# Kernel tuning notes

Measured on AMD Instinct MI355X. Metric: run time of the kernel, lower is better.

Reference implementation:

```python
import jax, jax.numpy as jnp
import numpy as np

DIM = 256
NUM_HEADS = 8
HEAD_DIM = DIM // NUM_HEADS
SCALE = float(HEAD_DIM) ** (-0.5)


def setup_inputs() -> dict:
    key = jax.random.key(0)
    ks = jax.random.split(key, 11)
    TGT, B = 2048, 4
    q = jax.random.normal(ks[0], (TGT, B, DIM), dtype=jnp.float32)
    k = jax.random.normal(ks[1], (TGT, B, DIM), dtype=jnp.float32)
    v = jax.random.normal(ks[2], (TGT, B, DIM), dtype=jnp.float32)
    init = 1.0 / np.sqrt(DIM)
    Wq = jax.random.uniform(ks[3], (DIM, DIM), jnp.float32, -init, init)
    bq = jax.random.uniform(ks[4], (DIM,), jnp.float32, -init, init)
    Wk = jax.random.uniform(ks[5], (DIM, DIM), jnp.float32, -init, init)
    bk = jax.random.uniform(ks[6], (DIM,), jnp.float32, -init, init)
    Wv = jax.random.uniform(ks[7], (DIM, DIM), jnp.float32, -init, init)
    bv = jax.random.uniform(ks[8], (DIM,), jnp.float32, -init, init)
    Wp = jax.random.uniform(ks[9], (DIM, DIM), jnp.float32, -init, init)
    bp = jax.random.uniform(ks[10], (DIM,), jnp.float32, -init, init)
    return {"q": q, "k": k, "v": v, "Wq": Wq, "bq": bq, "Wk": Wk, "bk": bk,
            "Wv": Wv, "bv": bv, "Wp": Wp, "bp": bp}


def reference(q, k, v, Wq, bq, Wk, bk, Wv, bv, Wp, bp):
    tgt_len, bsz, embed_dim = q.shape
    src_len = k.shape[0]
    # NOTE: original scales q BEFORE the q projection (faithful to source).
    qp = (q * SCALE) @ Wq.T + bq                      # [T, B, D]
    kp = k @ Wk.T + bk                                # [S, B, D]
    vp = v @ Wv.T + bv                                # [S, B, D]
    # reshape to (B*H, len, head_dim) like view + transpose(0,1)
    qh = qp.reshape(tgt_len, bsz * NUM_HEADS, HEAD_DIM).transpose(1, 0, 2)
    kh = kp.reshape(src_len, bsz * NUM_HEADS, HEAD_DIM).transpose(1, 0, 2)
    vh = vp.reshape(src_len, bsz * NUM_HEADS, HEAD_DIM).transpose(1, 0, 2)
    attn = jnp.einsum('bqd,bkd->bqk', qh, kh)         # [B*H, T, S]
    attn = jax.nn.softmax(attn, axis=-1)
    out = jnp.einsum('bqk,bkd->bqd', attn, vh)        # [B*H, T, hd]
    out = out.transpose(1, 0, 2).reshape(tgt_len, bsz, embed_dim)
    out = out @ Wp.T + bp                             # output projection
    return out
```

## Files before the change

### kernel.cpp

```cpp
#include <hip/hip_runtime.h>
#include <hip/hip_bf16.h>

#define T_LEN 2048
#define BSZ 4
#define EMB 256
#define HDIM 32
#define QSCALE 0.17677669529663687f
#define LOG2E 1.4426950408889634f

using bf16x8 = __attribute__((ext_vector_type(8))) short;
using bf16x4 = __attribute__((ext_vector_type(4))) short;
using f32x4 = __attribute__((ext_vector_type(4))) float;

static __device__ __forceinline__ unsigned fasu(float f) {
  union { float f; unsigned u; } c; c.f = f; return c.u;
}
static __device__ __forceinline__ unsigned pack2r(float lo, float hi) {
  return __builtin_amdgcn_perm(fasu(hi) + 0x8000u, fasu(lo) + 0x8000u, 0x07060302u);
}
static __device__ __forceinline__ unsigned short bfr(float x) {
  return (unsigned short)((fasu(x) + 0x8000u) >> 16);
}

__global__ __launch_bounds__(256) void cvt_w4(const float* __restrict__ s0, const float* __restrict__ s1,
                                              const float* __restrict__ s2, const float* __restrict__ s3,
                                              unsigned* __restrict__ d0, unsigned* __restrict__ d1,
                                              unsigned* __restrict__ d2, unsigned* __restrict__ d3) {
  const float* src = blockIdx.y == 0 ? s0 : blockIdx.y == 1 ? s1 : blockIdx.y == 2 ? s2 : s3;
  unsigned* dst = blockIdx.y == 0 ? d0 : blockIdx.y == 1 ? d1 : blockIdx.y == 2 ? d2 : d3;
  int i = blockIdx.x * 256 + threadIdx.x;
  float4 v = ((const float4*)src)[i];
  uint2 o; o.x = pack2r(v.x, v.y); o.y = pack2r(v.z, v.w);
  ((uint2*)dst)[i] = o;
}

__global__ __launch_bounds__(256) void qkv_proj(
    const float* __restrict__ Aq, const float* __restrict__ Ak, const float* __restrict__ Av,
    const unsigned short* __restrict__ Wq, const unsigned short* __restrict__ Wk, const unsigned short* __restrict__ Wv,
    const float* __restrict__ bq, const float* __restrict__ bk, const float* __restrict__ bv,
    unsigned short* __restrict__ qh, unsigned short* __restrict__ kh, unsigned short* __restrict__ vt) {
  __shared__ __align__(16) unsigned short smem[64 * 72];
  const int z = blockIdx.z;
  const float* A = z == 0 ? Aq : z == 1 ? Ak : Av;
  const unsigned short* W = z == 0 ? Wq : z == 1 ? Wk : Wv;
  const float* bias = z == 0 ? bq : z == 1 ? bk : bv;
  const float ascale = z == 0 ? QSCALE * LOG2E : 1.0f;
  const float bscale = z == 0 ? LOG2E : 1.0f;
  const int lane = threadIdx.x & 63;
  const int wave = threadIdx.x >> 6;
  const int quad = lane >> 4;
  const int l16 = lane & 15;
  const int m0b = blockIdx.x * 64;
  const int m0 = m0b + wave * 16;
  const int n0 = blockIdx.y * 64;
  f32x4 acc0 = {0.f, 0.f, 0.f, 0.f}, acc1 = acc0, acc2 = acc0, acc3 = acc0;
  const float* arow = A + (m0 + l16) * EMB;
#pragma unroll
  for (int k0 = 0; k0 < EMB; k0 += 32) {
    const float4* ap = (const float4*)(arow + k0 + quad * 8);
    float4 a0 = ap[0], a1 = ap[1];
    union { unsigned u[4]; bf16x8 v; } af;
    af.u[0] = pack2r(a0.x * ascale, a0.y * ascale);
    af.u[1] = pack2r(a0.z * ascale, a0.w * ascale);
    af.u[2] = pack2r(a1.x * ascale, a1.y * ascale);
    af.u[3] = pack2r(a1.z * ascale, a1.w * ascale);
    const unsigned short* wbase = W + k0 + quad * 8;
    bf16x8 b0 = *(const bf16x8*)(wbase + (n0 + 0 + l16) * EMB);
    bf16x8 b1 = *(const bf16x8*)(wbase + (n0 + 16 + l16) * EMB);
    bf16x8 b2 = *(const bf16x8*)(wbase + (n0 + 32 + l16) * EMB);
    bf16x8 b3 = *(const bf16x8*)(wbase + (n0 + 48 + l16) * EMB);
    acc0 = __builtin_amdgcn_mfma_f32_16x16x32_bf16(af.v, b0, acc0, 0, 0, 0);
    acc1 = __builtin_amdgcn_mfma_f32_16x16x32_bf16(af.v, b1, acc1, 0, 0, 0);
    acc2 = __builtin_amdgcn_mfma_f32_16x16x32_bf16(af.v, b2, acc2, 0, 0, 0);
    acc3 = __builtin_amdgcn_mfma_f32_16x16x32_bf16(af.v, b3, acc3, 0, 0, 0);
  }
  f32x4 accs[4] = {acc0, acc1, acc2, acc3};
#pragma unroll
  for (int nt = 0; nt < 4; ++nt) {
    float bn = bias[n0 + nt * 16 + l16] * bscale;
#pragma unroll
    for (int r = 0; r < 4; ++r)
      smem[(wave * 16 + quad * 4 + r) * 72 + nt * 16 + l16] = bfr(accs[nt][r] + bn);
  }
  __syncthreads();
  if (z < 2) {
    int row = threadIdx.x >> 2, seg = threadIdx.x & 3;
    int m = m0b + row, t = m >> 2, b = m & 3;
    int n = n0 + seg * 16, h = n >> 5, hd = n & 31;
    unsigned short* dst = (z == 0 ? qh : kh) + (((b << 3) + h) * T_LEN + t) * HDIM + hd;
    *(bf16x8*)(dst + 0) = *(const bf16x8*)(smem + row * 72 + seg * 16 + 0);
    *(bf16x8*)(dst + 8) = *(const bf16x8*)(smem + row * 72 + seg * 16 + 8);
  } else {
    int n = threadIdx.x >> 2, b = threadIdx.x & 3;
    unsigned w[8];
#pragma unroll
    for (int i = 0; i < 8; ++i) {
      unsigned lo = smem[((2 * i) * 4 + b) * 72 + n];
      unsigned hi = smem[((2 * i + 1) * 4 + b) * 72 + n];
      w[i] = lo | (hi << 16);
    }
    int nf = n0 + n, h = nf >> 5, hd = nf & 31;
    int tbase = m0b >> 2;
    unsigned* base = (unsigned*)(vt + (((b << 3) + h) * HDIM + hd) * T_LEN + tbase);
    ((uint4*)base)[0] = make_uint4(w[0], w[1], w[2], w[3]);
    ((uint4*)base)[1] = make_uint4(w[4], w[5], w[6], w[7]);
  }
}

__global__ __launch_bounds__(256) void out_gemm(const unsigned short* __restrict__ A,
                                                const unsigned short* __restrict__ W,
                                                const float* __restrict__ bias,
                                                float* __restrict__ out) {
  __shared__ __align__(16) float smem[64 * 68];
  const int lane = threadIdx.x & 63;
  const int wave = threadIdx.x >> 6;
  const int quad = lane >> 4;
  const int l16 = lane & 15;
  const int m0b = blockIdx.x * 64;
  const int m0 = m0b + wave * 16;
  const int n0 = blockIdx.y * 64;
  f32x4 acc0 = {0.f, 0.f, 0.f, 0.f}, acc1 = acc0, acc2 = acc0, acc3 = acc0;
  const unsigned short* arow = A + (m0 + l16) * EMB;
#pragma unroll
  for (int k0 = 0; k0 < EMB; k0 += 32) {
    bf16x8 af = *(const bf16x8*)(arow + k0 + quad * 8);
    const unsigned short* wbase = W + k0 + quad * 8;
    bf16x8 b0 = *(const bf16x8*)(wbase + (n0 + 0 + l16) * EMB);
    bf16x8 b1 = *(const bf16x8*)(wbase + (n0 + 16 + l16) * EMB);
    bf16x8 b2 = *(const bf16x8*)(wbase + (n0 + 32 + l16) * EMB);
    bf16x8 b3 = *(const bf16x8*)(wbase + (n0 + 48 + l16) * EMB);
    acc0 = __builtin_amdgcn_mfma_f32_16x16x32_bf16(af, b0, acc0, 0, 0, 0);
    acc1 = __builtin_amdgcn_mfma_f32_16x16x32_bf16(af, b1, acc1, 0, 0, 0);
    acc2 = __builtin_amdgcn_mfma_f32_16x16x32_bf16(af, b2, acc2, 0, 0, 0);
    acc3 = __builtin_amdgcn_mfma_f32_16x16x32_bf16(af, b3, acc3, 0, 0, 0);
  }
  f32x4 accs[4] = {acc0, acc1, acc2, acc3};
#pragma unroll
  for (int nt = 0; nt < 4; ++nt) {
    float bn = bias[n0 + nt * 16 + l16];
#pragma unroll
    for (int r = 0; r < 4; ++r)
      smem[(wave * 16 + quad * 4 + r) * 68 + nt * 16 + l16] = accs[nt][r] + bn;
  }
  __syncthreads();
  int row = threadIdx.x >> 2, seg = threadIdx.x & 3;
  const float4* srcp = (const float4*)(smem + row * 68 + seg * 16);
  float4* dstp = (float4*)(out + (m0b + row) * EMB + n0 + seg * 16);
#pragma unroll
  for (int i = 0; i < 4; ++i) dstp[i] = srcp[i];
}

__global__ __launch_bounds__(256) void flash_attn(const unsigned short* __restrict__ qh,
                                                  const unsigned short* __restrict__ kh,
                                                  const unsigned short* __restrict__ vt,
                                                  unsigned short* __restrict__ aout) {
  __shared__ __align__(16) unsigned short kbuf[2][128 * 32];
  __shared__ __align__(16) unsigned short vbuf[2][32 * 136];
  const int tid = threadIdx.x;
  const int lane = tid & 63;
  const int wave = tid >> 6;
  const int quad = lane >> 4;
  const int l16 = lane & 15;
  const int bh = blockIdx.x;
  const int q0 = blockIdx.y * 128 + wave * 32;
  const unsigned short* qs = qh + bh * (T_LEN * HDIM);
  const unsigned short* ks = kh + bh * (T_LEN * HDIM);
  const unsigned short* vs = vt + bh * (T_LEN * HDIM);
  const bf16x8 qf0 = *(const bf16x8*)(qs + (q0 + l16) * HDIM + quad * 8);
  const bf16x8 qf1 = *(const bf16x8*)(qs + (q0 + 16 + l16) * HDIM + quad * 8);
  f32x4 o00 = {0.f, 0.f, 0.f, 0.f};
  f32x4 o01 = o00, o10 = o00, o11 = o00, la0 = o00, la1 = o00;
  const f32x4 zero = o00;
  bf16x4 ones;
  ones[0] = ones[1] = ones[2] = ones[3] = (short)0x3F80;

  const int vrow = tid >> 4;
  const int vcol = (tid & 15) * 8;

  {
    uint4 ka = *(const uint4*)(ks + tid * 8);
    uint4 kb = *(const uint4*)(ks + (tid + 256) * 8);
    uint4 va = *(const uint4*)(vs + vrow * T_LEN + vcol);
    uint4 vb = *(const uint4*)(vs + (vrow + 16) * T_LEN + vcol);
    *(uint4*)(&kbuf[0][tid * 8]) = ka;
    *(uint4*)(&kbuf[0][(tid + 256) * 8]) = kb;
    *(uint4*)(&vbuf[0][vrow * 136 + vcol]) = va;
    *(uint4*)(&vbuf[0][(vrow + 16) * 136 + vcol]) = vb;
  }
  __syncthreads();

  for (int chunk = 0; chunk < 16; ++chunk) {
    const int buf = chunk & 1;
    uint4 ka, kb, va, vb;
    const bool pf = (chunk + 1) < 16;
    if (pf) {
      const int kk0 = (chunk + 1) * 128;
      const unsigned short* kg = ks + kk0 * HDIM;
      ka = *(const uint4*)(kg + tid * 8);
      kb = *(const uint4*)(kg + (tid + 256) * 8);
      va = *(const uint4*)(vs + vrow * T_LEN + kk0 + vcol);
      vb = *(const uint4*)(vs + (vrow + 16) * T_LEN + kk0 + vcol);
    }
#pragma unroll
    for (int it = 0; it < 8; ++it) {
      const int kkl = it * 16;
      bf16x8 kf = *(const bf16x8*)(&kbuf[buf][(kkl + l16) * 32 + quad * 8]);
      bf16x4 vfa = *(const bf16x4*)(&vbuf[buf][l16 * 136 + kkl + quad * 4]);
      bf16x4 vfb = *(const bf16x4*)(&vbuf[buf][(l16 + 16) * 136 + kkl + quad * 4]);
      f32x4 s0 = __builtin_amdgcn_mfma_f32_16x16x32_bf16(kf, qf0, zero, 0, 0, 0);
      f32x4 s1 = __builtin_amdgcn_mfma_f32_16x16x32_bf16(kf, qf1, zero, 0, 0, 0);
      union { unsigned u[2]; bf16x4 v; } pp0, pp1;
      {
        float a = __builtin_amdgcn_exp2f(s0[0]), b = __builtin_amdgcn_exp2f(s0[1]);
        float c = __builtin_amdgcn_exp2f(s0[2]), d = __builtin_amdgcn_exp2f(s0[3]);
        pp0.u[0] = pack2r(a, b); pp0.u[1] = pack2r(c, d);
        a = __builtin_amdgcn_exp2f(s1[0]); b = __builtin_amdgcn_exp2f(s1[1]);
        c = __builtin_amdgcn_exp2f(s1[2]); d = __builtin_amdgcn_exp2f(s1[3]);
        pp1.u[0] = pack2r(a, b); pp1.u[1] = pack2r(c, d);
      }
      o00 = __builtin_amdgcn_mfma_f32_16x16x16bf16_1k(vfa, pp0.v, o00, 0, 0, 0);
      o01 = __builtin_amdgcn_mfma_f32_16x16x16bf16_1k(vfb, pp0.v, o01, 0, 0, 0);
      la0 = __builtin_amdgcn_mfma_f32_16x16x16bf16_1k(ones, pp0.v, la0, 0, 0, 0);
      o10 = __builtin_amdgcn_mfma_f32_16x16x16bf16_1k(vfa, pp1.v, o10, 0, 0, 0);
      o11 = __builtin_amdgcn_mfma_f32_16x16x16bf16_1k(vfb, pp1.v, o11, 0, 0, 0);
      la1 = __builtin_amdgcn_mfma_f32_16x16x16bf16_1k(ones, pp1.v, la1, 0, 0, 0);
    }
    if (pf) {
      const int nb = buf ^ 1;
      *(uint4*)(&kbuf[nb][tid * 8]) = ka;
      *(uint4*)(&kbuf[nb][(tid + 256) * 8]) = kb;
      *(uint4*)(&vbuf[nb][vrow * 136 + vcol]) = va;
      *(uint4*)(&vbuf[nb][(vrow + 16) * 136 + vcol]) = vb;
    }
    __syncthreads();
  }

  const int srcA = l16 + ((quad & 1) << 5);
  const int srcB = srcA + 16;
  const bool lowq = quad < 2;
  const int b = bh >> 3, h = bh & 7;
#pragma unroll
  for (int f = 0; f < 2; ++f) {
    f32x4 oh0 = f == 0 ? o00 : o10;
    f32x4 oh1 = f == 0 ? o01 : o11;
    const float inv = 1.f / (f == 0 ? la0[0] : la1[0]);
    unsigned oa = pack2r(oh0[0] * inv, oh0[1] * inv), ob = pack2r(oh0[2] * inv, oh0[3] * inv);
    unsigned oc = pack2r(oh1[0] * inv, oh1[1] * inv), od = pack2r(oh1[2] * inv, oh1[3] * inv);
    union { unsigned u[4]; bf16x8 v; } of;
    unsigned ta, tc;
    ta = __shfl(oa, srcA); tc = __shfl(oc, srcA); of.u[0] = lowq ? ta : tc;
    ta = __shfl(ob, srcA); tc = __shfl(od, srcA); of.u[1] = lowq ? ta : tc;
    ta = __shfl(oa, srcB); tc = __shfl(oc, srcB); of.u[2] = lowq ? ta : tc;
    ta = __shfl(ob, srcB); tc = __shfl(od, srcB); of.u[3] = lowq ? ta : tc;
    const int t = q0 + f * 16 + l16;
    *(bf16x8*)(aout + (t * BSZ + b) * EMB + h * HDIM + quad * 8) = of.v;
  }
}

extern "C" void kernel_launch(void* const* d_in, const int* in_sizes, int n_in,
                              void* d_out, int out_size, void* d_ws, size_t ws_size,
                              hipStream_t stream) {
  const float* q  = (const float*)d_in[0];
  const float* k  = (const float*)d_in[1];
  const float* v  = (const float*)d_in[2];
  const float* Wq = (const float*)d_in[3];
  const float* bq = (const float*)d_in[4];
  const float* Wk = (const float*)d_in[5];
  const float* bk = (const float*)d_in[6];
  const float* Wv = (const float*)d_in[7];
  const float* bv = (const float*)d_in[8];
  const float* Wp = (const float*)d_in[9];
  const float* bp = (const float*)d_in[10];
  float* out = (float*)d_out;

  char* ws = (char*)d_ws;
  unsigned short* qh   = (unsigned short*)(ws);
  unsigned short* kh   = (unsigned short*)(ws + (4u << 20));
  unsigned short* vt   = (unsigned short*)(ws + (8u << 20));
  unsigned short* aout = (unsigned short*)(ws + (12u << 20));
  unsigned short* wqb  = (unsigned short*)(ws + (16u << 20));
  unsigned short* wkb  = wqb + 65536;
  unsigned short* wvb  = wqb + 2 * 65536;
  unsigned short* wpb  = wqb + 3 * 65536;

  cvt_w4<<<dim3(64, 4), 256, 0, stream>>>(Wq, Wk, Wv, Wp,
                                          (unsigned*)wqb, (unsigned*)wkb,
                                          (unsigned*)wvb, (unsigned*)wpb);
  qkv_proj<<<dim3(128, 4, 3), 256, 0, stream>>>(q, k, v, wqb, wkb, wvb, bq, bk, bv, qh, kh, vt);
  flash_attn<<<dim3(32, 16), 256, 0, stream>>>(qh, kh, vt, aout);
  out_gemm<<<dim3(128, 4), 256, 0, stream>>>(aout, wpb, bp, out);
}
```

Measured before the change: 166.8 us.

## Split attention over key halves and add a combine kernel

```diff
diff --git a/kernel.cpp b/kernel.cpp
--- a/kernel.cpp
+++ b/kernel.cpp
@@ -153,7 +153,8 @@
 __global__ __launch_bounds__(256) void flash_attn(const unsigned short* __restrict__ qh,
                                                   const unsigned short* __restrict__ kh,
                                                   const unsigned short* __restrict__ vt,
-                                                  unsigned short* __restrict__ aout) {
+                                                  float* __restrict__ po,
+                                                  float* __restrict__ pl) {
   __shared__ __align__(16) unsigned short kbuf[2][128 * 32];
   __shared__ __align__(16) unsigned short vbuf[2][32 * 136];
   const int tid = threadIdx.x;
@@ -162,7 +163,9 @@
   const int quad = lane >> 4;
   const int l16 = lane & 15;
   const int bh = blockIdx.x;
+  const int split = blockIdx.z;
   const int q0 = blockIdx.y * 128 + wave * 32;
+  const int kbeg = split * 1024;
   const unsigned short* qs = qh + bh * (T_LEN * HDIM);
   const unsigned short* ks = kh + bh * (T_LEN * HDIM);
   const unsigned short* vs = vt + bh * (T_LEN * HDIM);
@@ -178,10 +181,11 @@
   const int vcol = (tid & 15) * 8;
 
   {
-    uint4 ka = *(const uint4*)(ks + tid * 8);
-    uint4 kb = *(const uint4*)(ks + (tid + 256) * 8);
-    uint4 va = *(const uint4*)(vs + vrow * T_LEN + vcol);
-    uint4 vb = *(const uint4*)(vs + (vrow + 16) * T_LEN + vcol);
+    const unsigned short* kg = ks + kbeg * HDIM;
+    uint4 ka = *(const uint4*)(kg + tid * 8);
+    uint4 kb = *(const uint4*)(kg + (tid + 256) * 8);
+    uint4 va = *(const uint4*)(vs + vrow * T_LEN + kbeg + vcol);
+    uint4 vb = *(const uint4*)(vs + (vrow + 16) * T_LEN + kbeg + vcol);
     *(uint4*)(&kbuf[0][tid * 8]) = ka;
     *(uint4*)(&kbuf[0][(tid + 256) * 8]) = kb;
     *(uint4*)(&vbuf[0][vrow * 136 + vcol]) = va;
@@ -189,12 +193,12 @@
   }
   __syncthreads();
 
-  for (int chunk = 0; chunk < 16; ++chunk) {
+  for (int chunk = 0; chunk < 8; ++chunk) {
     const int buf = chunk & 1;
     uint4 ka, kb, va, vb;
-    const bool pf = (chunk + 1) < 16;
+    const bool pf = (chunk + 1) < 8;
     if (pf) {
-      const int kk0 = (chunk + 1) * 128;
+      const int kk0 = kbeg + (chunk + 1) * 128;
       const unsigned short* kg = ks + kk0 * HDIM;
       ka = *(const uint4*)(kg + tid * 8);
       kb = *(const uint4*)(kg + (tid + 256) * 8);
@@ -235,26 +239,38 @@
     __syncthreads();
   }
 
-  const int srcA = l16 + ((quad & 1) << 5);
-  const int srcB = srcA + 16;
-  const bool lowq = quad < 2;
-  const int b = bh >> 3, h = bh & 7;
+  const int base = (split * 32 + bh) * T_LEN;
 #pragma unroll
   for (int f = 0; f < 2; ++f) {
-    f32x4 oh0 = f == 0 ? o00 : o10;
-    f32x4 oh1 = f == 0 ? o01 : o11;
-    const float inv = 1.f / (f == 0 ? la0[0] : la1[0]);
-    unsigned oa = pack2r(oh0[0] * inv, oh0[1] * inv), ob = pack2r(oh0[2] * inv, oh0[3] * inv);
-    unsigned oc = pack2r(oh1[0] * inv, oh1[1] * inv), od = pack2r(oh1[2] * inv, oh1[3] * inv);
-    union { unsigned u[4]; bf16x8 v; } of;
-    unsigned ta, tc;
-    ta = __shfl(oa, srcA); tc = __shfl(oc, srcA); of.u[0] = lowq ? ta : tc;
-    ta = __shfl(ob, srcA); tc = __shfl(od, srcA); of.u[1] = lowq ? ta : tc;
-    ta = __shfl(oa, srcB); tc = __shfl(oc, srcB); of.u[2] = lowq ? ta : tc;
-    ta = __shfl(ob, srcB); tc = __shfl(od, srcB); of.u[3] = lowq ? ta : tc;
     const int t = q0 + f * 16 + l16;
-    *(bf16x8*)(aout + (t * BSZ + b) * EMB + h * HDIM + quad * 8) = of.v;
-  }
+    float* dst = po + (base + t) * 32 + quad * 4;
+    *(f32x4*)dst = (f == 0 ? o00 : o10);
+    *(f32x4*)(dst + 16) = (f == 0 ? o01 : o11);
+    if (quad == 0) pl[base + t] = (f == 0 ? la0 : la1)[0];
+  }
+}
+
+__global__ __launch_bounds__(256) void combine(const float* __restrict__ po,
+                                               const float* __restrict__ pl,
+                                               unsigned short* __restrict__ aout) {
+  const int r = threadIdx.x >> 5;
+  const int c = (threadIdx.x & 31) * 8;
+  const int row = blockIdx.x * 8 + r;
+  const int t = row >> 2, b = row & 3;
+  const int h = c >> 5, d = c & 31;
+  const int bh = b * 8 + h;
+  const float* p0 = po + (bh * T_LEN + t) * 32 + d;
+  const float* p1 = po + ((32 + bh) * T_LEN + t) * 32 + d;
+  const float inv = 1.f / (pl[bh * T_LEN + t] + pl[(32 + bh) * T_LEN + t]);
+  float4 a0 = *(const float4*)p0, a1 = *(const float4*)(p0 + 4);
+  float4 b0 = *(const float4*)p1, b1 = *(const float4*)(p1 + 4);
+  uint2 o[2];
+  o[0].x = pack2r((a0.x + b0.x) * inv, (a0.y + b0.y) * inv);
+  o[0].y = pack2r((a0.z + b0.z) * inv, (a0.w + b0.w) * inv);
+  o[1].x = pack2r((a1.x + b1.x) * inv, (a1.y + b1.y) * inv);
+  o[1].y = pack2r((a1.z + b1.z) * inv, (a1.w + b1.w) * inv);
+  *(uint2*)(aout + row * EMB + c) = o[0];
+  *(uint2*)(aout + row * EMB + c + 4) = o[1];
 }
 
 extern "C" void kernel_launch(void* const* d_in, const int* in_sizes, int n_in,
@@ -282,11 +298,14 @@
   unsigned short* wkb  = wqb + 65536;
   unsigned short* wvb  = wqb + 2 * 65536;
   unsigned short* wpb  = wqb + 3 * 65536;
+  float* po = (float*)(ws + (20u << 20));
+  float* pl = (float*)(ws + (36u << 20));
 
   cvt_w4<<<dim3(64, 4), 256, 0, stream>>>(Wq, Wk, Wv, Wp,
                                           (unsigned*)wqb, (unsigned*)wkb,
                                           (unsigned*)wvb, (unsigned*)wpb);
   qkv_proj<<<dim3(128, 4, 3), 256, 0, stream>>>(q, k, v, wqb, wkb, wvb, bq, bk, bv, qh, kh, vt);
-  flash_attn<<<dim3(32, 16), 256, 0, stream>>>(qh, kh, vt, aout);
+  flash_attn<<<dim3(32, 16, 2), 256, 0, stream>>>(qh, kh, vt, po, pl);
+  combine<<<1024, 256, 0, stream>>>(po, pl, aout);
   out_gemm<<<dim3(128, 4), 256, 0, stream>>>(aout, wpb, bp, out);
 }
```

Result: slower. 172.0 us (+3.1%).
